# Kernel tuning notes

Hardware: AMD Instinct MI355X
Metric: run time of the kernel (lower is better)

The kernel has to match this reference:

```python
import jax, jax.numpy as jnp
import numpy as np

B, N, IN_FT, OUT_FT = 1, 8192, 512, 256


def setup_inputs() -> dict:
    key = jax.random.key(0)
    k1, k2, k3, k4 = jax.random.split(key, 4)
    features = jax.random.normal(k1, (B, N, IN_FT), dtype=jnp.float32)
    adj = jax.random.uniform(k2, (B, N, N), dtype=jnp.float32)
    aug_adj1 = jax.random.uniform(k3, (B, N, N), dtype=jnp.float32)
    # Linear weight (xavier uniform), no bias on the Linear itself
    limit = float(np.sqrt(6.0 / (IN_FT + OUT_FT)))
    W = jax.random.uniform(k4, (OUT_FT, IN_FT), dtype=jnp.float32, minval=-limit, maxval=limit)
    bias = jnp.zeros((OUT_FT,), dtype=jnp.float32)  # GCN bias, filled 0
    prelu_a = jnp.full((1,), 0.25, dtype=jnp.float32)  # PReLU default slope
    return {"features": features, "adj": adj, "aug_adj1": aug_adj1,
            "W": W, "bias": bias, "prelu_a": prelu_a, "sparse": 0}


def _prelu(x, a):
    return jnp.where(x >= 0, x, a * x)


def _gcn(features, adj, W, bias, prelu_a):
    # Linear (no bias): [B,N,in] x [out,in]^T -> [B,N,out]
    seq_fts = jnp.einsum('bni,oi->bno', features, W)
    # Dense adjacency aggregation: bmm(adj, seq_fts)
    out = jnp.einsum('bnm,bmo->bno', adj, seq_fts) + bias
    return _prelu(out, prelu_a)


def reference(features, adj, aug_adj1, W, bias, prelu_a, sparse):
    # sparse flag is static (0 -> dense bmm path)
    h_0 = _gcn(features, adj, W, bias, prelu_a)
    h_1 = _gcn(features, aug_adj1, W, bias, prelu_a)
    return (h_0, h_1)
```

## Files before the change

### kernel.cpp

```cpp
#include <hip/hip_runtime.h>

#define NROW 8192
#define INF  512
#define OUTF 256
#define M_ELEM (NROW * OUTF)
#define NSTEP 32

typedef __bf16 v8bf __attribute__((ext_vector_type(8)));
typedef __bf16 v4bf __attribute__((ext_vector_type(4)));
typedef float  v4f  __attribute__((ext_vector_type(4)));

__device__ __forceinline__ v8bf cvt_bf8(v4f u0, v4f u1) {
  v8bf v;
  v[0]=(__bf16)u0[0]; v[1]=(__bf16)u0[1]; v[2]=(__bf16)u0[2]; v[3]=(__bf16)u0[3];
  v[4]=(__bf16)u1[0]; v[5]=(__bf16)u1[1]; v[6]=(__bf16)u1[2]; v[7]=(__bf16)u1[3];
  return v;
}

__global__ __launch_bounds__(256) void seq_fts_kernel(
    const float* __restrict__ feat, const float* __restrict__ W,
    __bf16* __restrict__ Bp) {
  const int tid  = threadIdx.x;
  const int lane = tid & 63, w = tid >> 6;
  const int llo  = lane & 15, lhi = lane >> 4;
  const int row0 = blockIdx.x * 64;
  const int col0 = w * 64;

  v4f acc[4][4] = {};
#pragma unroll 1
  for (int kb = 0; kb < INF / 32; ++kb) {
    const int kofs = kb * 32 + lhi * 8;
    v8bf a[4], b[4];
#pragma unroll
    for (int i = 0; i < 4; ++i) {
      const float* p = feat + (size_t)(row0 + i * 16 + llo) * INF + kofs;
      a[i] = cvt_bf8(*(const v4f*)p, *(const v4f*)(p + 4));
    }
#pragma unroll
    for (int i = 0; i < 4; ++i) {
      const float* p = W + (size_t)(col0 + i * 16 + llo) * INF + kofs;
      b[i] = cvt_bf8(*(const v4f*)p, *(const v4f*)(p + 4));
    }
#pragma unroll
    for (int ri = 0; ri < 4; ++ri)
#pragma unroll
      for (int ci = 0; ci < 4; ++ci)
        acc[ri][ci] = __builtin_amdgcn_mfma_f32_16x16x32_bf16(
            a[ri], b[ci], acc[ri][ci], 0, 0, 0);
  }
#pragma unroll
  for (int ri = 0; ri < 4; ++ri)
#pragma unroll
    for (int ci = 0; ci < 4; ++ci) {
      const int mf = row0 + ri * 16 + lhi * 4;
      const int o  = col0 + ci * 16 + llo;
      size_t e = (((size_t)(mf >> 5) * 16 + (o >> 4)) * 64 +
                  ((mf >> 3) & 3) * 16 + (o & 15)) * 8 + (mf & 7);
      v4bf v;
      v[0] = (__bf16)acc[ri][ci][0]; v[1] = (__bf16)acc[ri][ci][1];
      v[2] = (__bf16)acc[ri][ci][2]; v[3] = (__bf16)acc[ri][ci][3];
      *(v4bf*)(Bp + e) = v;
    }
}

__global__ __launch_bounds__(512, 2)
__attribute__((amdgpu_waves_per_eu(2, 2)))
void gcn_agg_kernel(
    const float* __restrict__ adjA, const float* __restrict__ adjB,
    const __bf16* __restrict__ Bp, const float* __restrict__ bias,
    const float* __restrict__ prelu_a, float* __restrict__ out) {
  const int tid  = threadIdx.x;
  const int lane = tid & 63, w = tid >> 6;
  const int llo  = lane & 15, lhi = lane >> 4;
  const int row0 = blockIdx.x * 64;
  const int z    = blockIdx.y;
  const float* __restrict__ adj = z ? adjB : adjA;

  __shared__ __align__(16) char LdsA[2][65536];

  v4f acc[4][2] = {};

  v4f areg[8];
  auto issue_a = [&](int t) {
#pragma unroll
    for (int i = 0; i < 8; ++i) {
      const int r = w * 8 + i;
      const float* src =
          adj + (size_t)(row0 + r) * NROW + t * 256 + (lane << 2);
      areg[i] = __builtin_nontemporal_load((const v4f*)src);
    }
  };
  auto write_a = [&](int buf) {
#pragma unroll
    for (int i = 0; i < 8; ++i) {
      const int r   = w * 8 + i;
      const int key = ((r & 15) << 1) | ((r >> 3) & 1);
      *(v4f*)(&LdsA[buf][r * 1024 + ((lane ^ key) << 4)]) = areg[i];
    }
  };

  const __bf16* __restrict__ Bpw = Bp + ((size_t)(w * 2) * 64 + lane) * 8;
  auto load_bg = [&](int t, int g, v8bf (&bb)[2]) {
#pragma unroll
    for (int ci = 0; ci < 2; ++ci)
      bb[ci] = *(const v8bf*)(
          Bpw + ((size_t)((t * 8 + g) * 16 + ci)) * 512);
  };

  auto compute_g = [&](int buf, int kg, v8bf (&bb)[2]) {
    const char* ab = &LdsA[buf][0];
    v8bf af[4];
#pragma unroll
    for (int rt = 0; rt < 4; ++rt) {
      const int r   = rt * 16 + llo;
      const int key = ((r & 15) << 1) | ((r >> 3) & 1);
      const char* base = ab + r * 1024;
      v4f u0 = *(const v4f*)(base + (((kg * 8 + lhi * 2    ) ^ key) << 4));
      v4f u1 = *(const v4f*)(base + (((kg * 8 + lhi * 2 + 1) ^ key) << 4));
      af[rt] = cvt_bf8(u0, u1);
    }
#pragma unroll
    for (int ci = 0; ci < 2; ++ci)
#pragma unroll
      for (int rt = 0; rt < 4; ++rt)
        acc[rt][ci] = __builtin_amdgcn_mfma_f32_16x16x32_bf16(
            af[rt], bb[ci], acc[rt][ci], 0, 0, 0);
  };

  issue_a(0);
  asm volatile("s_waitcnt vmcnt(0)" ::: "memory");
  write_a(0);
  asm volatile("s_waitcnt lgkmcnt(0)" ::: "memory");
  __builtin_amdgcn_s_barrier();

  v8bf b[2][2];
#pragma unroll 1
  for (int t = 0; t < NSTEP; ++t) {
    load_bg(t, 0, b[0]);
    __builtin_amdgcn_sched_barrier(0);
    load_bg(t, 1, b[1]);
    __builtin_amdgcn_sched_barrier(0);
    if (t + 1 < NSTEP) issue_a(t + 1);
    __builtin_amdgcn_sched_barrier(0);
#pragma unroll
    for (int kg = 0; kg < 8; ++kg) {
      compute_g(t & 1, kg, b[kg & 1]);
      if (kg + 2 < 8) {
        __builtin_amdgcn_sched_barrier(0);
        load_bg(t, kg + 2, b[kg & 1]);
        __builtin_amdgcn_sched_barrier(0);
      }
    }
    __builtin_amdgcn_sched_barrier(0);
    if (t + 1 < NSTEP) {
      asm volatile("s_waitcnt vmcnt(0)" ::: "memory");
      write_a((t + 1) & 1);
      asm volatile("s_waitcnt lgkmcnt(0)" ::: "memory");
    }
    __builtin_amdgcn_s_barrier();
  }

  const float slope = prelu_a[0];
  float* __restrict__ outp = out + (size_t)z * M_ELEM;
#pragma unroll
  for (int ci = 0; ci < 2; ++ci) {
    const int o  = w * 32 + ci * 16 + llo;
    const float bs = bias[o];
#pragma unroll
    for (int rt = 0; rt < 4; ++rt) {
      const int m = row0 + rt * 16 + lhi * 4;
#pragma unroll
      for (int r = 0; r < 4; ++r) {
        float v = acc[rt][ci][r] + bs;
        outp[(size_t)(m + r) * OUTF + o] = v >= 0.f ? v : slope * v;
      }
    }
  }
}

extern "C" void kernel_launch(void* const* d_in, const int* in_sizes, int n_in,
                              void* d_out, int out_size, void* d_ws, size_t ws_size,
                              hipStream_t stream) {
  const float* feat = (const float*)d_in[0];
  const float* adj  = (const float*)d_in[1];
  const float* aug  = (const float*)d_in[2];
  const float* W    = (const float*)d_in[3];
  const float* bias = (const float*)d_in[4];
  const float* pa   = (const float*)d_in[5];
  float* out = (float*)d_out;
  __bf16* Bp = (__bf16*)d_ws;

  seq_fts_kernel<<<dim3(NROW / 64), 256, 0, stream>>>(feat, W, Bp);
  gcn_agg_kernel<<<dim3(NROW / 64, 2), 512, 0, stream>>>(
      adj, aug, Bp, bias, pa, out);
}
```

Measured before the change: 176.8 us.

## Use 128-row aggregation tiles with split-K partials and separate bias/PReLU reduce

The aggregation kernel now gives each block 128 adjacency rows and a 128-wide K slice per step, and splits the K dimension into S chunks across a new grid dimension. Each chunk writes fp32 partial sums to workspace, and a new reduce kernel sums them and applies bias and PReLU. The larger row tile is meant to halve the repeated reads of the bf16 seq_fts operand per adjacency row while keeping the block count the same. The cost is extra partial-sum write and read traffic, a third kernel launch, and narrower 8-byte per-lane adjacency loads.

```diff
diff --git a/kernel.cpp b/kernel.cpp
--- a/kernel.cpp
+++ b/kernel.cpp
@@ -4,11 +4,11 @@
 #define INF  512
 #define OUTF 256
 #define M_ELEM (NROW * OUTF)
-#define NSTEP 32
 
 typedef __bf16 v8bf __attribute__((ext_vector_type(8)));
 typedef __bf16 v4bf __attribute__((ext_vector_type(4)));
 typedef float  v4f  __attribute__((ext_vector_type(4)));
+typedef float  v2f  __attribute__((ext_vector_type(2)));
 
 __device__ __forceinline__ v8bf cvt_bf8(v4f u0, v4f u1) {
   v8bf v;
@@ -67,35 +67,39 @@
 __attribute__((amdgpu_waves_per_eu(2, 2)))
 void gcn_agg_kernel(
     const float* __restrict__ adjA, const float* __restrict__ adjB,
-    const __bf16* __restrict__ Bp, const float* __restrict__ bias,
-    const float* __restrict__ prelu_a, float* __restrict__ out) {
+    const __bf16* __restrict__ Bp, float* __restrict__ P,
+    int S, int nsteps) {
   const int tid  = threadIdx.x;
   const int lane = tid & 63, w = tid >> 6;
   const int llo  = lane & 15, lhi = lane >> 4;
-  const int row0 = blockIdx.x * 64;
-  const int z    = blockIdx.y;
+  const int row0 = blockIdx.x * 128;
+  const int y    = blockIdx.y;
+  const int z    = blockIdx.z;
   const float* __restrict__ adj = z ? adjB : adjA;
+  const int k0   = y * nsteps * 128;
+  const int kk0  = y * nsteps * 4;
 
   __shared__ __align__(16) char LdsA[2][65536];
 
-  v4f acc[4][2] = {};
-
-  v4f areg[8];
+  v4f acc[8][2] = {};
+
+  v2f areg[16];
   auto issue_a = [&](int t) {
 #pragma unroll
-    for (int i = 0; i < 8; ++i) {
-      const int r = w * 8 + i;
+    for (int i = 0; i < 16; ++i) {
+      const int r = w * 16 + i;
       const float* src =
-          adj + (size_t)(row0 + r) * NROW + t * 256 + (lane << 2);
-      areg[i] = __builtin_nontemporal_load((const v4f*)src);
+          adj + (size_t)(row0 + r) * NROW + k0 + t * 128 + (lane << 1);
+      areg[i] = __builtin_nontemporal_load((const v2f*)src);
     }
   };
   auto write_a = [&](int buf) {
 #pragma unroll
-    for (int i = 0; i < 8; ++i) {
-      const int r   = w * 8 + i;
+    for (int i = 0; i < 16; ++i) {
+      const int r   = w * 16 + i;
       const int key = ((r & 15) << 1) | ((r >> 3) & 1);
-      *(v4f*)(&LdsA[buf][r * 1024 + ((lane ^ key) << 4)]) = areg[i];
+      const int byt = r * 512 + ((((lane >> 1) ^ key) << 4) | ((lane & 1) << 3));
+      *(v2f*)(&LdsA[buf][byt]) = areg[i];
     }
   };
 
@@ -104,25 +108,26 @@
 #pragma unroll
     for (int ci = 0; ci < 2; ++ci)
       bb[ci] = *(const v8bf*)(
-          Bpw + ((size_t)((t * 8 + g) * 16 + ci)) * 512);
+          Bpw + ((size_t)((kk0 + t * 4 + g) * 16 + ci)) * 512);
   };
 
   auto compute_g = [&](int buf, int kg, v8bf (&bb)[2]) {
     const char* ab = &LdsA[buf][0];
-    v8bf af[4];
-#pragma unroll
-    for (int rt = 0; rt < 4; ++rt) {
+    v8bf af[8];
+#pragma unroll
+    for (int rt = 0; rt < 8; ++rt) {
       const int r   = rt * 16 + llo;
       const int key = ((r & 15) << 1) | ((r >> 3) & 1);
-      const char* base = ab + r * 1024;
-      v4f u0 = *(const v4f*)(base + (((kg * 8 + lhi * 2    ) ^ key) << 4));
-      v4f u1 = *(const v4f*)(base + (((kg * 8 + lhi * 2 + 1) ^ key) << 4));
+      const char* base = ab + r * 512;
+      const int s0 = kg * 8 + lhi * 2;
+      v4f u0 = *(const v4f*)(base + (((s0    ) ^ key) << 4));
+      v4f u1 = *(const v4f*)(base + (((s0 + 1) ^ key) << 4));
       af[rt] = cvt_bf8(u0, u1);
     }
 #pragma unroll
     for (int ci = 0; ci < 2; ++ci)
 #pragma unroll
-      for (int rt = 0; rt < 4; ++rt)
+      for (int rt = 0; rt < 8; ++rt)
         acc[rt][ci] = __builtin_amdgcn_mfma_f32_16x16x32_bf16(
             af[rt], bb[ci], acc[rt][ci], 0, 0, 0);
   };
@@ -135,24 +140,24 @@
 
   v8bf b[2][2];
 #pragma unroll 1
-  for (int t = 0; t < NSTEP; ++t) {
+  for (int t = 0; t < nsteps; ++t) {
     load_bg(t, 0, b[0]);
     __builtin_amdgcn_sched_barrier(0);
     load_bg(t, 1, b[1]);
     __builtin_amdgcn_sched_barrier(0);
-    if (t + 1 < NSTEP) issue_a(t + 1);
-    __builtin_amdgcn_sched_barrier(0);
-#pragma unroll
-    for (int kg = 0; kg < 8; ++kg) {
+    if (t + 1 < nsteps) issue_a(t + 1);
+    __builtin_amdgcn_sched_barrier(0);
+#pragma unroll
+    for (int kg = 0; kg < 4; ++kg) {
       compute_g(t & 1, kg, b[kg & 1]);
-      if (kg + 2 < 8) {
+      if (kg + 2 < 4) {
         __builtin_amdgcn_sched_barrier(0);
         load_bg(t, kg + 2, b[kg & 1]);
         __builtin_amdgcn_sched_barrier(0);
       }
     }
     __builtin_amdgcn_sched_barrier(0);
-    if (t + 1 < NSTEP) {
+    if (t + 1 < nsteps) {
       asm volatile("s_waitcnt vmcnt(0)" ::: "memory");
       write_a((t + 1) & 1);
       asm volatile("s_waitcnt lgkmcnt(0)" ::: "memory");
@@ -160,21 +165,38 @@
     __builtin_amdgcn_s_barrier();
   }
 
+  float* __restrict__ Pp = P + (size_t)(z * S + y) * M_ELEM;
+#pragma unroll
+  for (int ci = 0; ci < 2; ++ci) {
+    const int o = w * 32 + ci * 16 + llo;
+#pragma unroll
+    for (int rt = 0; rt < 8; ++rt) {
+      const int m = row0 + rt * 16 + lhi * 4;
+#pragma unroll
+      for (int r = 0; r < 4; ++r)
+        Pp[(size_t)(m + r) * OUTF + o] = acc[rt][ci][r];
+    }
+  }
+}
+
+__global__ __launch_bounds__(256) void reduce_kernel(
+    const float* __restrict__ P, const float* __restrict__ bias,
+    const float* __restrict__ prelu_a, float* __restrict__ out, int S) {
   const float slope = prelu_a[0];
-  float* __restrict__ outp = out + (size_t)z * M_ELEM;
-#pragma unroll
-  for (int ci = 0; ci < 2; ++ci) {
-    const int o  = w * 32 + ci * 16 + llo;
-    const float bs = bias[o];
-#pragma unroll
-    for (int rt = 0; rt < 4; ++rt) {
-      const int m = row0 + rt * 16 + lhi * 4;
-#pragma unroll
-      for (int r = 0; r < 4; ++r) {
-        float v = acc[rt][ci][r] + bs;
-        outp[(size_t)(m + r) * OUTF + o] = v >= 0.f ? v : slope * v;
-      }
-    }
+  const int nv4 = 2 * M_ELEM / 4;
+  for (int v = blockIdx.x * 256 + threadIdx.x; v < nv4; v += gridDim.x * 256) {
+    const int z = v >> 19;
+    const size_t r = (size_t)(v & 524287) * 4;
+    const int o = (int)(r & 255);
+    v4f s = {};
+    for (int yy = 0; yy < S; ++yy)
+      s += *(const v4f*)(P + (size_t)(z * S + yy) * M_ELEM + r);
+    v4f b4 = *(const v4f*)(bias + o);
+    s += b4;
+    v4f res;
+#pragma unroll
+    for (int i = 0; i < 4; ++i) res[i] = s[i] >= 0.f ? s[i] : slope * s[i];
+    *(v4f*)(out + (size_t)z * M_ELEM + r) = res;
   }
 }
 
@@ -190,7 +212,13 @@
   float* out = (float*)d_out;
   __bf16* Bp = (__bf16*)d_ws;
 
+  const size_t MB = 1ull << 20;
+  int S = (ws_size >= 4 * MB + 2 * 2 * (size_t)M_ELEM * 4) ? 2 : 1;
+  float* P = (S == 1) ? out : (float*)((char*)d_ws + 4 * MB);
+  const int nsteps = NROW / 128 / S;
+
   seq_fts_kernel<<<dim3(NROW / 64), 256, 0, stream>>>(feat, W, Bp);
-  gcn_agg_kernel<<<dim3(NROW / 64, 2), 512, 0, stream>>>(
-      adj, aug, Bp, bias, pa, out);
-}
+  gcn_agg_kernel<<<dim3(NROW / 128, S, 2), 512, 0, stream>>>(
+      adj, aug, Bp, P, S, nsteps);
+  reduce_kernel<<<dim3(1024), 256, 0, stream>>>(P, bias, pa, out, S);
+}
```

After: 190.4 us. 1.08x slower.
